# Optimization experiments

Hardware: AMD Instinct MI355X
Metric: run time of the kernel (lower is better)

## Reference

```python
import math
import jax, jax.numpy as jnp
import numpy as np

H = 16  # num_attention_heads
EPS = 1e-6

def _rmsnorm(x, w):
    xf = x.astype(jnp.float32)
    y = xf * jax.lax.rsqrt(jnp.mean(xf * xf, axis=-1, keepdims=True) + EPS)
    return (y * w).astype(x.dtype)

def setup_inputs() -> dict:
    key = jax.random.key(0)
    ks = jax.random.split(key, 4)
    B, S, D = 4, 1536, 2048
    return {
        "x": jax.random.normal(ks[0], (B, S, D), jnp.float32),
        "w_qkv": jax.random.normal(ks[1], (D, 3 * D), jnp.float32) * (1.0 / math.sqrt(D)),
        "b_qkv": jnp.zeros((3 * D,), jnp.float32),
        "q_ln_w": jnp.ones((D,), jnp.float32),
        "k_ln_w": jnp.ones((D,), jnp.float32),
        "w_out": jax.random.normal(ks[2], (D, D), jnp.float32) * (1.0 / math.sqrt(D)),
        "b_out": jnp.zeros((D,), jnp.float32),
    }

def reference(x, w_qkv, b_qkv, q_ln_w, k_ln_w, w_out, b_out):
    B, S, D = x.shape
    hd = D // H
    scale = 1.0 / math.sqrt(hd)
    qkv = x @ w_qkv + b_qkv                     # [B,S,3D]
    q, k, v = jnp.split(qkv, 3, axis=-1)
    q = _rmsnorm(q, q_ln_w)                     # QK-RMSNorm over hidden dim
    k = _rmsnorm(k, k_ln_w)
    # [B,S,D] -> [B,H,S,hd]
    q = q.reshape(B, S, H, hd).transpose(0, 2, 1, 3)
    k = k.reshape(B, S, H, hd).transpose(0, 2, 1, 3)
    v = v.reshape(B, S, H, hd).transpose(0, 2, 1, 3)
    scores = jnp.einsum('bhqd,bhkd->bhqk', q, k) * scale
    min_val = jnp.finfo(scores.dtype).min
    causal = jnp.tril(jnp.ones((S, S), dtype=bool))
    scores = jnp.where(causal[None, None], scores, min_val)
    probs = jax.nn.softmax(scores, axis=-1)
    out = jnp.einsum('bhqk,bhkd->bhqd', probs, v)
    out = out.transpose(0, 2, 1, 3).reshape(B, S, D)
    return out @ w_out + b_out
```

## Files before the change

### kernel.cpp

```cpp
#include <hip/hip_runtime.h>
#include <stdint.h>

#define BB 4
#define SS 1536
#define DD 2048
#define HH 16
#define HD 128
#define BS (BB * SS)
#define N3 (3 * DD)

typedef __bf16 bf16x8 __attribute__((ext_vector_type(8)));
typedef float f32x4 __attribute__((ext_vector_type(4)));

__device__ __forceinline__ void async16(const void* g, void* lds) {
  __builtin_amdgcn_global_load_lds(
      (const __attribute__((address_space(1))) unsigned int*)g,
      (__attribute__((address_space(3))) unsigned int*)lds, 16, 0, 0);
}

__global__ __launch_bounds__(256) void cast_bf16_kernel(
    const float* __restrict__ in, __bf16* __restrict__ out) {
  long i = ((long)blockIdx.x * 256 + threadIdx.x) * 8;
  float4 a = *(const float4*)(in + i);
  float4 b = *(const float4*)(in + i + 4);
  bf16x8 o;
  o[0] = (__bf16)a.x; o[1] = (__bf16)a.y; o[2] = (__bf16)a.z; o[3] = (__bf16)a.w;
  o[4] = (__bf16)b.x; o[5] = (__bf16)b.y; o[6] = (__bf16)b.z; o[7] = (__bf16)b.w;
  *(bf16x8*)(out + i) = o;
}

__global__ __launch_bounds__(256) void transpose_cast_kernel(
    const float* __restrict__ in, __bf16* __restrict__ out, int R, int C) {
  __shared__ __bf16 t[32][33];
  int tx = threadIdx.x & 31, ty = threadIdx.x >> 5;
  long r0 = (long)blockIdx.y * 32, c0 = (long)blockIdx.x * 32;
#pragma unroll
  for (int i = 0; i < 4; ++i)
    t[ty + i * 8][tx] = (__bf16)in[(r0 + ty + i * 8) * C + c0 + tx];
  __syncthreads();
#pragma unroll
  for (int i = 0; i < 4; ++i)
    out[(c0 + ty + i * 8) * R + r0 + tx] = t[tx][ty + i * 8];
}

__device__ __forceinline__ void store_val(__bf16* p, float v) { *p = (__bf16)v; }
__device__ __forceinline__ void store_val(float* p, float v) { *p = v; }

template <typename OutT>
__global__ __launch_bounds__(256, 2) void gemm_bt_kernel(
    const __bf16* __restrict__ A, const __bf16* __restrict__ Bt,
    const float* __restrict__ bias, OutT* __restrict__ C,
    int M, int N, int K) {
  __shared__ __attribute__((aligned(16))) __bf16 sA[128 * 32];
  __shared__ __attribute__((aligned(16))) __bf16 sB[128 * 32];
  const int tid = threadIdx.x;
  const int wave = tid >> 6, lane = tid & 63;
  const int quad = lane >> 4, l15 = lane & 15;
  const int bm = blockIdx.y * 128, bn = blockIdx.x * 128;
  const int wr = (wave >> 1) * 64, wc = (wave & 1) * 64;

  const int srow = lane >> 2;
  const int scol = ((lane & 3) ^ ((lane >> 3) & 3)) * 8;
  const __bf16* Ap = A + (long)(bm + wave * 32 + srow) * K + scol;
  const __bf16* Bp = Bt + (long)(bn + wave * 32 + srow) * K + scol;
  __bf16* sAw = &sA[wave * 32 * 32];
  __bf16* sBw = &sB[wave * 32 * 32];

  const int achunk = (quad ^ ((l15 >> 1) & 3)) * 8;

  f32x4 acc[4][4] = {};

  for (int k0 = 0; k0 < K; k0 += 32) {
    __syncthreads();
    async16(Ap + k0, sAw);
    async16(Ap + k0 + (long)16 * K, sAw + 16 * 32);
    async16(Bp + k0, sBw);
    async16(Bp + k0 + (long)16 * K, sBw + 16 * 32);
    __syncthreads();
    bf16x8 af[4], bfr[4];
#pragma unroll
    for (int i = 0; i < 4; ++i)
      af[i] = *(const bf16x8*)&sA[(wr + i * 16 + l15) * 32 + achunk];
#pragma unroll
    for (int i = 0; i < 4; ++i)
      bfr[i] = *(const bf16x8*)&sB[(wc + i * 16 + l15) * 32 + achunk];
#pragma unroll
    for (int i = 0; i < 4; ++i)
#pragma unroll
      for (int j = 0; j < 4; ++j)
        acc[i][j] = __builtin_amdgcn_mfma_f32_16x16x32_bf16(af[i], bfr[j],
                                                            acc[i][j], 0, 0, 0);
  }

#pragma unroll
  for (int i = 0; i < 4; ++i) {
    int row0 = bm + wr + i * 16 + quad * 4;
#pragma unroll
    for (int j = 0; j < 4; ++j) {
      int col = bn + wc + j * 16 + l15;
      float bv = bias[col];
#pragma unroll
      for (int r = 0; r < 4; ++r)
        store_val(&C[(long)(row0 + r) * N + col], acc[i][j][r] + bv);
    }
  }
}

__global__ __launch_bounds__(256) void rmsnorm_kernel(
    __bf16* __restrict__ qkv, const float* __restrict__ qw,
    const float* __restrict__ kw) {
  const int r = blockIdx.x;
  const bool isQ = r < BS;
  const int row = isQ ? r : r - BS;
  __bf16* p = qkv + (long)row * N3 + (isQ ? 0 : DD);
  const float* w = isQ ? qw : kw;
  const float extra = isQ ? (0.0883883476483184f * 1.44269504088896f) : 1.0f;
  const int t = threadIdx.x;

  bf16x8 v = *(const bf16x8*)(p + t * 8);
  float f[8];
  float s = 0.f;
#pragma unroll
  for (int i = 0; i < 8; ++i) { f[i] = (float)v[i]; s += f[i] * f[i]; }
#pragma unroll
  for (int off = 32; off > 0; off >>= 1) s += __shfl_xor(s, off, 64);
  __shared__ float red[4];
  if ((t & 63) == 0) red[t >> 6] = s;
  __syncthreads();
  float tot = red[0] + red[1] + red[2] + red[3];
  float rs = rsqrtf(tot * (1.0f / (float)DD) + 1e-6f) * extra;
  bf16x8 o;
#pragma unroll
  for (int i = 0; i < 8; ++i) o[i] = (__bf16)(f[i] * rs * w[t * 8 + i]);
  *(bf16x8*)(p + t * 8) = o;
}

__global__ __launch_bounds__(256) void transpose_v_kernel(
    const __bf16* __restrict__ qkv, __bf16* __restrict__ vt) {
  __shared__ __bf16 t[32][33];
  const int bh = blockIdx.z, b = bh >> 4, h = bh & 15;
  const int s0 = blockIdx.x * 32, d0 = blockIdx.y * 32;
  const int tx = threadIdx.x & 31, ty = threadIdx.x >> 5;
#pragma unroll
  for (int i = 0; i < 4; ++i) {
    int s = s0 + ty + i * 8;
    t[ty + i * 8][tx] =
        qkv[(long)(b * SS + s) * N3 + 2 * DD + h * HD + d0 + tx];
  }
  __syncthreads();
#pragma unroll
  for (int i = 0; i < 4; ++i) {
    int d = d0 + ty + i * 8;
    vt[((long)bh * HD + d) * SS + s0 + tx] = t[tx][ty + i * 8];
  }
}

__global__ __launch_bounds__(256, 2) void attn_kernel(
    const __bf16* __restrict__ qkv, const __bf16* __restrict__ vt,
    __bf16* __restrict__ O) {
  __shared__ __attribute__((aligned(16))) __bf16 sK[2][64 * 128];
  __shared__ __attribute__((aligned(16))) __bf16 sV[2][128 * 64];
  __shared__ __attribute__((aligned(16))) __bf16 sP[4][32 * 64];

  const int qi = gridDim.x - 1 - blockIdx.x, bh = blockIdx.y;
  const int b = bh >> 4, h = bh & 15;
  const int tid = threadIdx.x, wave = tid >> 6, lane = tid & 63;
  const int quad = lane >> 4, l15 = lane & 15;
  const int sw3 = l15 & 7;

  const long rowQ0 = (long)(b * SS + qi * 128);
  const int qrow0 = qi * 128 + wave * 32;
  const __bf16* kbase = qkv + (long)(b * SS) * N3 + DD + h * HD;
  const __bf16* vbase = vt + (long)bh * HD * SS;

  bf16x8 qf[2][4];
#pragma unroll
  for (int mt = 0; mt < 2; ++mt) {
    const __bf16* qp =
        qkv + (rowQ0 + wave * 32 + mt * 16 + l15) * N3 + h * HD + quad * 8;
#pragma unroll
    for (int kk = 0; kk < 4; ++kk) qf[mt][kk] = *(const bf16x8*)(qp + kk * 32);
  }

  f32x4 o_acc[2][8] = {};
  float l_acc[2][4] = {};

  __bf16* sPw = &sP[wave][0];
  const int jn = 2 * qi + 2;

  auto stageKV = [&](int j, int buf) {
#pragma unroll
    for (int t = 0; t < 4; ++t) {
      int rbase = wave * 16 + t * 4;
      int row = rbase + quad;
      const __bf16* src =
          kbase + (long)(j * 64 + row) * N3 + ((l15 ^ (row & 7)) * 8);
      async16(src, &sK[buf][rbase * 128]);
    }
#pragma unroll
    for (int t = 0; t < 4; ++t) {
      int rbase = wave * 32 + t * 8;
      int row = rbase + (lane >> 3);
      const __bf16* src = vbase + (long)row * SS + j * 64 +
                          (((lane & 7) ^ (row & 7)) * 8);
      async16(src, &sV[buf][rbase * 64]);
    }
  };

  stageKV(0, 0);

  for (int j = 0; j < jn; ++j) {
    const int buf = j & 1;
    __syncthreads();
    if (j + 1 < jn) stageKV(j + 1, buf ^ 1);

    const bool active = !((j == 2 * qi + 1) && (wave < 2));
    if (active) {
      const bool needMask =
          ((j == 2 * qi) && (wave < 2)) || ((j == 2 * qi + 1) && (wave >= 2));

      f32x4 sacc[2][4];
#pragma unroll
      for (int nt = 0; nt < 4; ++nt) {
        sacc[0][nt] = (f32x4){0.f, 0.f, 0.f, 0.f};
        sacc[1][nt] = (f32x4){0.f, 0.f, 0.f, 0.f};
#pragma unroll
        for (int kk = 0; kk < 4; ++kk) {
          bf16x8 bk = *(const bf16x8*)
              &sK[buf][(nt * 16 + l15) * 128 + (((kk * 4 + quad) ^ sw3) * 8)];
          sacc[0][nt] = __builtin_amdgcn_mfma_f32_16x16x32_bf16(
              qf[0][kk], bk, sacc[0][nt], 0, 0, 0);
          sacc[1][nt] = __builtin_amdgcn_mfma_f32_16x16x32_bf16(
              qf[1][kk], bk, sacc[1][nt], 0, 0, 0);
        }
      }
      if (needMask) {
#pragma unroll
        for (int mt = 0; mt < 2; ++mt) {
          int rowg0 = qrow0 + mt * 16 + quad * 4;
#pragma unroll
          for (int nt = 0; nt < 4; ++nt) {
            int colg = j * 64 + nt * 16 + l15;
#pragma unroll
            for (int r = 0; r < 4; ++r)
              if (colg > rowg0 + r) sacc[mt][nt][r] = -1e30f;
          }
        }
      }
#pragma unroll
      for (int mt = 0; mt < 2; ++mt) {
#pragma unroll
        for (int nt = 0; nt < 4; ++nt) {
#pragma unroll
          for (int r = 0; r < 4; ++r) {
            float pv = exp2f(sacc[mt][nt][r]);
            l_acc[mt][r] += pv;
            int prow = mt * 16 + quad * 4 + r;
            int pcol = nt * 16 + l15;
            sPw[prow * 64 + (((pcol >> 3) ^ (prow & 7)) * 8) + (pcol & 7)] =
                (__bf16)pv;
          }
        }
      }
#pragma unroll
      for (int kk = 0; kk < 2; ++kk) {
        bf16x8 ap0 = *(const bf16x8*)
            &sPw[l15 * 64 + (((kk * 4 + quad) ^ sw3) * 8)];
        bf16x8 ap1 = *(const bf16x8*)
            &sPw[(16 + l15) * 64 + (((kk * 4 + quad) ^ sw3) * 8)];
#pragma unroll
        for (int dt = 0; dt < 8; ++dt) {
          bf16x8 bv = *(const bf16x8*)
              &sV[buf][(dt * 16 + l15) * 64 + (((kk * 4 + quad) ^ sw3) * 8)];
          o_acc[0][dt] = __builtin_amdgcn_mfma_f32_16x16x32_bf16(
              ap0, bv, o_acc[0][dt], 0, 0, 0);
          o_acc[1][dt] = __builtin_amdgcn_mfma_f32_16x16x32_bf16(
              ap1, bv, o_acc[1][dt], 0, 0, 0);
        }
      }
    }
  }

#pragma unroll
  for (int mt = 0; mt < 2; ++mt) {
    __bf16* obase = O + (rowQ0 + wave * 32 + mt * 16 + quad * 4) * DD + h * HD;
#pragma unroll
    for (int r = 0; r < 4; ++r) {
      float l = l_acc[mt][r];
#pragma unroll
      for (int off = 1; off < 16; off <<= 1) l += __shfl_xor(l, off, 64);
      float inv = 1.0f / l;
#pragma unroll
      for (int dt = 0; dt < 8; ++dt)
        obase[(long)r * DD + dt * 16 + l15] = (__bf16)(o_acc[mt][dt][r] * inv);
    }
  }
}

extern "C" void kernel_launch(void* const* d_in, const int* in_sizes, int n_in,
                              void* d_out, int out_size, void* d_ws,
                              size_t ws_size, hipStream_t stream) {
  const float* x      = (const float*)d_in[0];
  const float* w_qkv  = (const float*)d_in[1];
  const float* b_qkv  = (const float*)d_in[2];
  const float* q_ln_w = (const float*)d_in[3];
  const float* k_ln_w = (const float*)d_in[4];
  const float* w_out  = (const float*)d_in[5];
  const float* b_out  = (const float*)d_in[6];
  float* out = (float*)d_out;

  char* w = (char*)d_ws;
  __bf16* xb    = (__bf16*)(w);
  __bf16* wqkvT = (__bf16*)(w + 25165824L);
  __bf16* woutT = (__bf16*)(w + 50331648L);
  __bf16* qkvb  = (__bf16*)(w + 58720256L);
  __bf16* vtb   = (__bf16*)(w + 134217728L);
  __bf16* atto  = xb;

  cast_bf16_kernel<<<dim3(BS * DD / 2048), 256, 0, stream>>>(x, xb);
  transpose_cast_kernel<<<dim3(N3 / 32, DD / 32), 256, 0, stream>>>(
      w_qkv, wqkvT, DD, N3);
  transpose_cast_kernel<<<dim3(DD / 32, DD / 32), 256, 0, stream>>>(
      w_out, woutT, DD, DD);

  gemm_bt_kernel<__bf16><<<dim3(N3 / 128, BS / 128), 256, 0, stream>>>(
      xb, wqkvT, b_qkv, qkvb, BS, N3, DD);

  rmsnorm_kernel<<<dim3(2 * BS), 256, 0, stream>>>(qkvb, q_ln_w, k_ln_w);

  transpose_v_kernel<<<dim3(SS / 32, HD / 32, BB * HH), 256, 0, stream>>>(
      qkvb, vtb);

  attn_kernel<<<dim3(SS / 128, BB * HH), 256, 0, stream>>>(qkvb, vtb, atto);

  gemm_bt_kernel<float><<<dim3(DD / 128, BS / 128), 256, 0, stream>>>(
      atto, woutT, b_out, out, BS, DD, DD);
}
```

Measured before the change: 535.3 us.

## Replace GEMM with 256x256 tile, double-buffered, interleaved load/MFMA schedule

```diff
diff --git a/kernel.cpp b/kernel.cpp
--- a/kernel.cpp
+++ b/kernel.cpp
@@ -46,58 +46,161 @@
 __device__ __forceinline__ void store_val(__bf16* p, float v) { *p = (__bf16)v; }
 __device__ __forceinline__ void store_val(float* p, float v) { *p = v; }
 
+#define MFMA_PRE()                                          \
+  __builtin_amdgcn_s_barrier();                             \
+  asm volatile("s_waitcnt lgkmcnt(0)" ::: "memory");        \
+  __builtin_amdgcn_sched_barrier(0);                        \
+  __builtin_amdgcn_s_setprio(1)
+#define MFMA_POST()                                         \
+  __builtin_amdgcn_s_setprio(0);                            \
+  __builtin_amdgcn_s_barrier()
+#define MFMA16(AF, BF, IOFF, JOFF)                                          \
+  _Pragma("unroll") for (int i_ = 0; i_ < 4; ++i_)                          \
+  _Pragma("unroll") for (int j_ = 0; j_ < 2; ++j_)                          \
+  _Pragma("unroll") for (int kk_ = 0; kk_ < 2; ++kk_)                       \
+    acc[(IOFF) + i_][(JOFF) + j_] = __builtin_amdgcn_mfma_f32_16x16x32_bf16( \
+        AF[i_][kk_], BF[j_][kk_], acc[(IOFF) + i_][(JOFF) + j_], 0, 0, 0)
+
 template <typename OutT>
-__global__ __launch_bounds__(256, 2) void gemm_bt_kernel(
+__global__ __launch_bounds__(512, 2) void gemm256_kernel(
     const __bf16* __restrict__ A, const __bf16* __restrict__ Bt,
     const float* __restrict__ bias, OutT* __restrict__ C,
     int M, int N, int K) {
-  __shared__ __attribute__((aligned(16))) __bf16 sA[128 * 32];
-  __shared__ __attribute__((aligned(16))) __bf16 sB[128 * 32];
+  __shared__ __attribute__((aligned(16))) __bf16 sA[2][2][128 * 64];
+  __shared__ __attribute__((aligned(16))) __bf16 sB[2][2][128 * 64];
+
   const int tid = threadIdx.x;
   const int wave = tid >> 6, lane = tid & 63;
   const int quad = lane >> 4, l15 = lane & 15;
-  const int bm = blockIdx.y * 128, bn = blockIdx.x * 128;
-  const int wr = (wave >> 1) * 64, wc = (wave & 1) * 64;
-
-  const int srow = lane >> 2;
-  const int scol = ((lane & 3) ^ ((lane >> 3) & 3)) * 8;
-  const __bf16* Ap = A + (long)(bm + wave * 32 + srow) * K + scol;
-  const __bf16* Bp = Bt + (long)(bn + wave * 32 + srow) * K + scol;
-  __bf16* sAw = &sA[wave * 32 * 32];
-  __bf16* sBw = &sB[wave * 32 * 32];
-
-  const int achunk = (quad ^ ((l15 >> 1) & 3)) * 8;
-
-  f32x4 acc[4][4] = {};
-
-  for (int k0 = 0; k0 < K; k0 += 32) {
-    __syncthreads();
-    async16(Ap + k0, sAw);
-    async16(Ap + k0 + (long)16 * K, sAw + 16 * 32);
-    async16(Bp + k0, sBw);
-    async16(Bp + k0 + (long)16 * K, sBw + 16 * 32);
-    __syncthreads();
-    bf16x8 af[4], bfr[4];
-#pragma unroll
-    for (int i = 0; i < 4; ++i)
-      af[i] = *(const bf16x8*)&sA[(wr + i * 16 + l15) * 32 + achunk];
-#pragma unroll
-    for (int i = 0; i < 4; ++i)
-      bfr[i] = *(const bf16x8*)&sB[(wc + i * 16 + l15) * 32 + achunk];
-#pragma unroll
-    for (int i = 0; i < 4; ++i)
-#pragma unroll
-      for (int j = 0; j < 4; ++j)
-        acc[i][j] = __builtin_amdgcn_mfma_f32_16x16x32_bf16(af[i], bfr[j],
-                                                            acc[i][j], 0, 0, 0);
-  }
-
-#pragma unroll
-  for (int i = 0; i < 4; ++i) {
-    int row0 = bm + wr + i * 16 + quad * 4;
+  const int s7 = l15 & 7;
+  const int wm = wave >> 2, wn = wave & 3;
+
+  const int nwg = gridDim.x;
+  int wg = (int)blockIdx.x;
+  wg = (wg & 7) * (nwg >> 3) + (wg >> 3);
+  const int NB = N >> 8;
+  const int bm = (wg / NB) << 8;
+  const int bn = (wg % NB) << 8;
+
+  const int srow = lane >> 3;
+  const int schunk = (lane & 7) ^ srow;
+  const __bf16* aSrc[2][2];
+  const __bf16* bSrc[2][2];
+#pragma unroll
+  for (int h = 0; h < 2; ++h)
+#pragma unroll
+    for (int t8 = 0; t8 < 2; ++t8) {
+      int rl = wave * 16 + t8 * 8 + srow;
+      aSrc[h][t8] = A + (long)(bm + h * 128 + rl) * K + schunk * 8;
+      bSrc[h][t8] = Bt + (long)(bn + h * 128 + rl) * K + schunk * 8;
+    }
+
+  auto stageA = [&](int kt, int b, int h) {
+#pragma unroll
+    for (int t8 = 0; t8 < 2; ++t8)
+      async16(aSrc[h][t8] + kt * 64, &sA[b][h][(wave * 16 + t8 * 8) * 64]);
+  };
+  auto stageB = [&](int kt, int b, int h) {
+#pragma unroll
+    for (int t8 = 0; t8 < 2; ++t8)
+      async16(bSrc[h][t8] + kt * 64, &sB[b][h][(wave * 16 + t8 * 8) * 64]);
+  };
+  auto readA = [&](int b, int i, int kk) -> bf16x8 {
+    return *(const bf16x8*)&sA[b][wm]
+        [(i * 16 + l15) * 64 + (((kk * 4 + quad) ^ s7) * 8)];
+  };
+  auto readB = [&](int b, int j, int kk) -> bf16x8 {
+    return *(const bf16x8*)&sB[b][wn >> 1]
+        [((wn & 1) * 64 + j * 16 + l15) * 64 + (((kk * 4 + quad) ^ s7) * 8)];
+  };
+
+  f32x4 acc[8][4] = {};
+
+  stageA(0, 0, 0); stageA(0, 0, 1); stageB(0, 0, 0); stageB(0, 0, 1);
+  stageA(1, 1, 0); stageA(1, 1, 1); stageB(1, 1, 0);
+  asm volatile("s_waitcnt vmcnt(6)" ::: "memory");
+  __builtin_amdgcn_s_barrier();
+
+  const int NT = K >> 6;
+  bf16x8 af[4][2], af2[4][2], bf[2][2], bf2[2][2];
+
+#pragma unroll 1
+  for (int t = 0; t < NT; t += 2) {
+    const bool full = (t + 2) < NT;
+
+#pragma unroll
+    for (int i = 0; i < 4; ++i) { af[i][0] = readA(0, i, 0); af[i][1] = readA(0, i, 1); }
+#pragma unroll
+    for (int j = 0; j < 2; ++j) { bf[j][0] = readB(0, j, 0); bf[j][1] = readB(0, j, 1); }
+    stageB(t + 1, 1, 1);
+    MFMA_PRE();
+    MFMA16(af, bf, 0, 0);
+    MFMA_POST();
+
+#pragma unroll
+    for (int i = 0; i < 4; ++i) { af2[i][0] = readA(0, 4 + i, 0); af2[i][1] = readA(0, 4 + i, 1); }
+    MFMA_PRE();
+    MFMA16(af2, bf, 4, 0);
+    MFMA_POST();
+
+#pragma unroll
+    for (int j = 0; j < 2; ++j) { bf2[j][0] = readB(0, 2 + j, 0); bf2[j][1] = readB(0, 2 + j, 1); }
+    if (full) stageA(t + 2, 0, 0);
+    MFMA_PRE();
+    MFMA16(af2, bf2, 4, 2);
+    MFMA_POST();
+
+    if (full) {
+      stageA(t + 2, 0, 1);
+      stageB(t + 2, 0, 0);
+      asm volatile("s_waitcnt vmcnt(6)" ::: "memory");
+    } else {
+      asm volatile("s_waitcnt vmcnt(0)" ::: "memory");
+    }
+    MFMA_PRE();
+    MFMA16(af, bf2, 0, 2);
+    MFMA_POST();
+
+#pragma unroll
+    for (int i = 0; i < 4; ++i) { af[i][0] = readA(1, i, 0); af[i][1] = readA(1, i, 1); }
+#pragma unroll
+    for (int j = 0; j < 2; ++j) { bf[j][0] = readB(1, j, 0); bf[j][1] = readB(1, j, 1); }
+    if (full) stageB(t + 2, 0, 1);
+    MFMA_PRE();
+    MFMA16(af, bf, 0, 0);
+    MFMA_POST();
+
+#pragma unroll
+    for (int i = 0; i < 4; ++i) { af2[i][0] = readA(1, 4 + i, 0); af2[i][1] = readA(1, 4 + i, 1); }
+    MFMA_PRE();
+    MFMA16(af2, bf, 4, 0);
+    MFMA_POST();
+
+#pragma unroll
+    for (int j = 0; j < 2; ++j) { bf2[j][0] = readB(1, 2 + j, 0); bf2[j][1] = readB(1, 2 + j, 1); }
+    if (full) stageA(t + 3, 1, 0);
+    MFMA_PRE();
+    MFMA16(af2, bf2, 4, 2);
+    MFMA_POST();
+
+    if (full) {
+      stageA(t + 3, 1, 1);
+      stageB(t + 3, 1, 0);
+      asm volatile("s_waitcnt vmcnt(6)" ::: "memory");
+    } else {
+      asm volatile("s_waitcnt vmcnt(0)" ::: "memory");
+    }
+    MFMA_PRE();
+    MFMA16(af, bf2, 0, 2);
+    MFMA_POST();
+  }
+
+#pragma unroll
+  for (int i = 0; i < 8; ++i) {
+    int row0 = bm + wm * 128 + i * 16 + quad * 4;
 #pragma unroll
     for (int j = 0; j < 4; ++j) {
-      int col = bn + wc + j * 16 + l15;
+      int col = bn + wn * 64 + j * 16 + l15;
       float bv = bias[col];
 #pragma unroll
       for (int r = 0; r < 4; ++r)
@@ -323,7 +426,7 @@
   transpose_cast_kernel<<<dim3(DD / 32, DD / 32), 256, 0, stream>>>(
       w_out, woutT, DD, DD);
 
-  gemm_bt_kernel<__bf16><<<dim3(N3 / 128, BS / 128), 256, 0, stream>>>(
+  gemm256_kernel<__bf16><<<dim3((BS / 256) * (N3 / 256)), 512, 0, stream>>>(
       xb, wqkvT, b_qkv, qkvb, BS, N3, DD);
 
   rmsnorm_kernel<<<dim3(2 * BS), 256, 0, stream>>>(qkvb, q_ln_w, k_ln_w);
@@ -333,6 +436,6 @@
 
   attn_kernel<<<dim3(SS / 128, BB * HH), 256, 0, stream>>>(qkvb, vtb, atto);
 
-  gemm_bt_kernel<float><<<dim3(DD / 128, BS / 128), 256, 0, stream>>>(
+  gemm256_kernel<float><<<dim3((BS / 256) * (DD / 256)), 512, 0, stream>>>(
       atto, woutT, b_out, out, BS, DD, DD);
 }
```

Measured after the change: 551.5 us. 1.03x slower.
